# Optimization experiments

Hardware: AMD Instinct MI355X
Metric: run time of the kernel (lower is better)

The kernel has to match this reference:

```python
import jax, jax.numpy as jnp
import numpy as np
import math

IN_FEATURES = 4096
OUT_FEATURES = 4096
NUM_COMPONENTS = 256
TWO_PI = 2.0 * math.pi


def setup_inputs() -> dict:
    key = jax.random.key(0)
    k1, k2, k3, k4 = jax.random.split(key, 4)
    x = jax.random.normal(k1, (4096, IN_FEATURES), dtype=jnp.float32)
    mus = jax.random.uniform(k2, (NUM_COMPONENTS, 2), dtype=jnp.float32)
    log_vars = -3.0 - jax.random.uniform(k3, (NUM_COMPONENTS, 2), dtype=jnp.float32)
    weights = jax.random.uniform(k4, (NUM_COMPONENTS,), dtype=jnp.float32) / NUM_COMPONENTS
    return {"x": x, "mus": mus, "log_vars": log_vars, "weights": weights}


def reference(x, mus, log_vars, weights):
    in_features = x.shape[1]
    x_in_idx = jnp.linspace(0.0, 1.0, in_features, dtype=jnp.float32)    # [I]
    x_out_idx = jnp.linspace(0.0, 1.0, OUT_FEATURES, dtype=jnp.float32)  # [O]
    vars_ = jnp.exp(log_vars)  # [M, 2]

    # Input-side Gaussian basis, fused with 1/sqrt(2*pi*var) and component weight: [I, M]
    d_in = (x_in_idx[:, None] - mus[None, :, 0]) ** 2
    G_in = jnp.exp(-d_in / (2.0 * vars_[None, :, 0])) / jnp.sqrt(TWO_PI * vars_[None, :, 0]) * weights[None, :]
    C = x @ G_in  # [B, M]

    # Output-side Gaussian pdf (Normal(mu1, sigma1).log_prob(x_out).exp()): [M, O]
    d_out = (x_out_idx[None, :] - mus[:, 1:2]) ** 2
    G_out = jnp.exp(-d_out / (2.0 * vars_[:, 1:2])) / jnp.sqrt(TWO_PI * vars_[:, 1:2])

    x_out = (C @ G_out) / (in_features * jnp.sum(weights))  # [B, O]
    return x_out
```

## Files before the change

### kernel.cpp

```cpp
#include <hip/hip_runtime.h>
#include <hip/hip_bf16.h>
#include <math.h>

#define IN_FEAT 4096
#define OUT_FEAT 4096
#define NCOMP 256
#define BATCH 4096
#define TWO_PI_F 6.28318530717958647692f

typedef __attribute__((ext_vector_type(8))) short short8;
typedef __attribute__((ext_vector_type(8))) __bf16 bf16x8;
typedef __attribute__((ext_vector_type(4))) float f32x4;
typedef __attribute__((ext_vector_type(16))) float f32x16;

__device__ __forceinline__ ushort f2b(float f) {
  union { float f; unsigned u; } v; v.f = f;
  unsigned r = (v.u + 0x7fffu + ((v.u >> 16) & 1u)) >> 16;
  return (ushort)r;
}

__device__ __forceinline__ float b2f(short s) {
  union { unsigned u; float f; } v; v.u = ((unsigned)(ushort)s) << 16;
  return v.f;
}

__device__ __forceinline__ bf16x8 ld_frag(const void* p) {
  short8 s = *(const short8*)p;
  return __builtin_bit_cast(bf16x8, s);
}

__device__ __forceinline__ bf16x8 cvt8f(float4 a, float4 b) {
  bf16x8 r;
  r[0] = (__bf16)a.x; r[1] = (__bf16)a.y; r[2] = (__bf16)a.z; r[3] = (__bf16)a.w;
  r[4] = (__bf16)b.x; r[5] = (__bf16)b.y; r[6] = (__bf16)b.z; r[7] = (__bf16)b.w;
  return r;
}

__device__ __forceinline__ void gload_lds16(const void* g, void* l) {
  __builtin_amdgcn_global_load_lds(
      (const __attribute__((address_space(1))) void*)g,
      (__attribute__((address_space(3))) void*)l, 16, 0, 0);
}

__global__ __launch_bounds__(256) void prep_kernel(
    const float* __restrict__ mus, const float* __restrict__ lvs,
    const float* __restrict__ w,
    ushort* __restrict__ Gt, ushort* __restrict__ GoT) {
  int idx = blockIdx.x * 256 + threadIdx.x;
  if (idx < NCOMP * IN_FEAT) {
    int m = idx >> 12, i = idx & (IN_FEAT - 1);
    float v = expf(lvs[2 * m]);
    float d = (float)i * (1.0f / (IN_FEAT - 1)) - mus[2 * m];
    float g = expf(-d * d * (0.5f / v)) * rsqrtf(TWO_PI_F * v) * w[m];
    Gt[idx] = f2b(g);
  } else {
    idx -= NCOMP * IN_FEAT;
    int o = idx >> 8, m = idx & (NCOMP - 1);
    float v = expf(lvs[2 * m + 1]);
    float d = (float)o * (1.0f / (OUT_FEAT - 1)) - mus[2 * m + 1];
    float g = expf(-d * d * (0.5f / v)) * rsqrtf(TWO_PI_F * v);
    GoT[idx] = f2b(g);
  }
}

template<int NS>
__global__ __launch_bounds__(512, 2) void gemm1_kernel(
    const float* __restrict__ x, const ushort* __restrict__ Gt,
    ushort* __restrict__ Cpart) {
  constexpr int KR = IN_FEAT / NS;
  constexpr int NT = KR / 32;
  __shared__ __align__(16) ushort Bs[NT * 8192];
  const int tid = threadIdx.x, wid = tid >> 6, lane = tid & 63;
  const int l15 = lane & 15, q = lane >> 4;
  const int m0 = blockIdx.x * 256;
  const int kb0 = blockIdx.y * KR;

  {
    const int brow = lane >> 2;
    const int bsw = (((lane & 3) ^ ((lane >> 3) & 3)) << 3);
    #pragma unroll
    for (int i = 0; i < 16; ++i) {
      int idx = wid * 16 + i;
      int seg = idx >> 4, nf = idx & 15;
      gload_lds16(&Gt[(size_t)(nf * 16 + brow) * IN_FEAT + kb0 + seg * 32 + bsw],
                  &Bs[seg * 8192 + nf * 512]);
    }
  }

  const int rb0 = m0 + wid * 32;
  const int rb1 = rb0 + 16;
  const float* xa = &x[(size_t)(rb0 + l15) * IN_FEAT + kb0 + q * 8];
  const float* xb = &x[(size_t)(rb1 + l15) * IN_FEAT + kb0 + q * 8];

  float4 P[4][4];
  #pragma unroll
  for (int s = 0; s < 4; ++s) {
    P[s][0] = *(const float4*)(xa + s * 32);
    P[s][1] = *(const float4*)(xa + s * 32 + 4);
    P[s][2] = *(const float4*)(xb + s * 32);
    P[s][3] = *(const float4*)(xb + s * 32 + 4);
  }

  __syncthreads();

  f32x4 acc0[16] = {}, acc1[16] = {};
  const int fswz = (q << 4) ^ (((l15 >> 1) & 3) << 4);

  #pragma unroll
  for (int t = 0; t < NT; ++t) {
    bf16x8 af0 = cvt8f(P[t & 3][0], P[t & 3][1]);
    bf16x8 af1 = cvt8f(P[t & 3][2], P[t & 3][3]);
    if (t + 4 < NT) {
      P[t & 3][0] = *(const float4*)(xa + (t + 4) * 32);
      P[t & 3][1] = *(const float4*)(xa + (t + 4) * 32 + 4);
      P[t & 3][2] = *(const float4*)(xb + (t + 4) * 32);
      P[t & 3][3] = *(const float4*)(xb + (t + 4) * 32 + 4);
    }
    const char* sb = (const char*)Bs + t * 16384;
    #pragma unroll
    for (int nf = 0; nf < 16; ++nf) {
      bf16x8 bf = ld_frag(sb + (nf * 16 + l15) * 64 + fswz);
      acc0[nf] = __builtin_amdgcn_mfma_f32_16x16x32_bf16(af0, bf, acc0[nf], 0, 0, 0);
      acc1[nf] = __builtin_amdgcn_mfma_f32_16x16x32_bf16(af1, bf, acc1[nf], 0, 0, 0);
    }
  }

  ushort* Cp = Cpart + (size_t)blockIdx.y * ((size_t)BATCH * NCOMP);
  #pragma unroll
  for (int nf = 0; nf < 16; ++nf)
    #pragma unroll
    for (int r = 0; r < 4; ++r) {
      int col = nf * 16 + l15;
      Cp[(size_t)(rb0 + q * 4 + r) * NCOMP + col] = f2b(acc0[nf][r]);
      Cp[(size_t)(rb1 + q * 4 + r) * NCOMP + col] = f2b(acc1[nf][r]);
    }
}

template<int NS>
__global__ __launch_bounds__(256) void reduce_kernel(ushort* __restrict__ Cp) {
  size_t i = ((size_t)blockIdx.x * 256 + threadIdx.x) * 8;
  float s[8] = {};
  #pragma unroll
  for (int p = 0; p < NS; ++p) {
    short8 v = *(const short8*)&Cp[(size_t)p * BATCH * NCOMP + i];
    #pragma unroll
    for (int e = 0; e < 8; ++e) s[e] += b2f(v[e]);
  }
  short8 hh;
  #pragma unroll
  for (int e = 0; e < 8; ++e) hh[e] = (short)f2b(s[e]);
  *(short8*)&Cp[i] = hh;
}

__global__ __launch_bounds__(256, 4) void gemm2_kernel(
    const ushort* __restrict__ Cb, const ushort* __restrict__ GoT,
    const float* __restrict__ w, float* __restrict__ out) {
  __shared__ __align__(16) ushort lds[2 * 8192];
  const int tid = threadIdx.x, wid = tid >> 6, lane = tid & 63;
  const int m0 = blockIdx.y * 128, n0 = blockIdx.x * 128;
  const int wr = (wid >> 1) * 64, wc = (wid & 1) * 64;
  const int r32 = lane & 31, h = lane >> 5;

  float4 wv = *(const float4*)&w[lane * 4];
  float s = wv.x + wv.y + wv.z + wv.w;
  #pragma unroll
  for (int off = 32; off > 0; off >>= 1) s += __shfl_xor(s, off);
  const float scale = 1.0f / ((float)IN_FEAT * s);

  const int brow = lane >> 2;
  const int bswz = (((lane & 3) ^ ((lane >> 3) & 3)) << 3);
  const int sw0 = (h << 4) ^ (((r32 >> 1) & 3) << 4);

  f32x16 acc[2][2] = {};

  #define STAGE2(buf, k0)                                                    \
    _Pragma("unroll")                                                        \
    for (int q2 = 0; q2 < 2; ++q2) {                                         \
      int c = wid * 2 + q2;                                                  \
      int row = c * 16 + brow;                                               \
      gload_lds16(&Cb[(size_t)(m0 + row) * NCOMP + (k0) + bswz],             \
                  &lds[(buf) * 8192 + c * 512]);                             \
      gload_lds16(&GoT[(size_t)(n0 + row) * NCOMP + (k0) + bswz],            \
                  &lds[(buf) * 8192 + 4096 + c * 512]);                      \
    }

  STAGE2(0, 0)
  __syncthreads();

  for (int t = 0; t < 8; ++t) {
    if (t < 7) STAGE2((t + 1) & 1, (t + 1) * 32)
    const char* base = (const char*)lds + (t & 1) * 16384;
    const char* Bb = base + 8192;
    #pragma unroll
    for (int s2 = 0; s2 < 2; ++s2) {
      const int off = sw0 ^ (s2 << 5);
      bf16x8 a0 = ld_frag(base + (wr + r32) * 64 + off);
      bf16x8 a1 = ld_frag(base + (wr + 32 + r32) * 64 + off);
      bf16x8 b0 = ld_frag(Bb + (wc + r32) * 64 + off);
      bf16x8 b1 = ld_frag(Bb + (wc + 32 + r32) * 64 + off);
      acc[0][0] = __builtin_amdgcn_mfma_f32_32x32x16_bf16(a0, b0, acc[0][0], 0, 0, 0);
      acc[0][1] = __builtin_amdgcn_mfma_f32_32x32x16_bf16(a0, b1, acc[0][1], 0, 0, 0);
      acc[1][0] = __builtin_amdgcn_mfma_f32_32x32x16_bf16(a1, b0, acc[1][0], 0, 0, 0);
      acc[1][1] = __builtin_amdgcn_mfma_f32_32x32x16_bf16(a1, b1, acc[1][1], 0, 0, 0);
    }
    __syncthreads();
  }
  #undef STAGE2

  #pragma unroll
  for (int mi = 0; mi < 2; ++mi)
    #pragma unroll
    for (int nj = 0; nj < 2; ++nj)
      #pragma unroll
      for (int g = 0; g < 16; ++g) {
        int row = m0 + wr + mi * 32 + (g & 3) + 8 * (g >> 2) + 4 * h;
        int col = n0 + wc + nj * 32 + r32;
        out[(size_t)row * OUT_FEAT + col] = acc[mi][nj][g] * scale;
      }
}

extern "C" void kernel_launch(void* const* d_in, const int* in_sizes, int n_in,
                              void* d_out, int out_size, void* d_ws, size_t ws_size,
                              hipStream_t stream) {
  const float* x   = (const float*)d_in[0];
  const float* mus = (const float*)d_in[1];
  const float* lvs = (const float*)d_in[2];
  const float* w   = (const float*)d_in[3];
  float* out = (float*)d_out;

  ushort* Gt  = (ushort*)d_ws;
  ushort* GoT = Gt  + (size_t)NCOMP * IN_FEAT;
  ushort* Cpart = GoT + (size_t)OUT_FEAT * NCOMP;

  prep_kernel<<<(NCOMP * IN_FEAT + OUT_FEAT * NCOMP) / 256, 256, 0, stream>>>(
      mus, lvs, w, Gt, GoT);

  gemm1_kernel<16><<<dim3(BATCH / 256, 16), 512, 0, stream>>>(x, Gt, Cpart);
  reduce_kernel<16><<<BATCH * NCOMP / 8 / 256, 256, 0, stream>>>(Cpart);

  gemm2_kernel<<<dim3(OUT_FEAT / 128, BATCH / 128), 256, 0, stream>>>(
      Cpart, GoT, w, out);
}
```

Baseline: 65.19 us.

## Restructure gemm1 into 64-row tiles with fewer K splits and chunked B staging

The first GEMM now uses 64-row blocks, with each wave handling 16 rows and half of the 256 components. It loops over K in 256-wide chunks, staging G into LDS per chunk under barriers. The split-K factor drops from 16 to 4, or to 1 when the workspace is small, which cuts the partial-sum traffic and reduce work. The cost is less reuse of each staged G tile across rows and exposed load latency, since loads and compute are not double-buffered.

```diff
diff --git a/kernel.cpp b/kernel.cpp
--- a/kernel.cpp
+++ b/kernel.cpp
@@ -63,76 +63,70 @@
   }
 }
 
-template<int NS>
+template<int NSPLIT>
 __global__ __launch_bounds__(512, 2) void gemm1_kernel(
     const float* __restrict__ x, const ushort* __restrict__ Gt,
     ushort* __restrict__ Cpart) {
-  constexpr int KR = IN_FEAT / NS;
-  constexpr int NT = KR / 32;
-  __shared__ __align__(16) ushort Bs[NT * 8192];
+  constexpr int KR = IN_FEAT / NSPLIT;
+  constexpr int NSC = KR / 256;
+  __shared__ __align__(16) ushort Bs[8 * 8192];
   const int tid = threadIdx.x, wid = tid >> 6, lane = tid & 63;
   const int l15 = lane & 15, q = lane >> 4;
-  const int m0 = blockIdx.x * 256;
+  const int rg = wid >> 1, h2 = wid & 1;
+  const int m0 = blockIdx.x * 64;
   const int kb0 = blockIdx.y * KR;
 
-  {
-    const int brow = lane >> 2;
-    const int bsw = (((lane & 3) ^ ((lane >> 3) & 3)) << 3);
-    #pragma unroll
-    for (int i = 0; i < 16; ++i) {
-      int idx = wid * 16 + i;
-      int seg = idx >> 4, nf = idx & 15;
-      gload_lds16(&Gt[(size_t)(nf * 16 + brow) * IN_FEAT + kb0 + seg * 32 + bsw],
-                  &Bs[seg * 8192 + nf * 512]);
-    }
-  }
-
-  const int rb0 = m0 + wid * 32;
-  const int rb1 = rb0 + 16;
-  const float* xa = &x[(size_t)(rb0 + l15) * IN_FEAT + kb0 + q * 8];
-  const float* xb = &x[(size_t)(rb1 + l15) * IN_FEAT + kb0 + q * 8];
-
-  float4 P[4][4];
-  #pragma unroll
-  for (int s = 0; s < 4; ++s) {
-    P[s][0] = *(const float4*)(xa + s * 32);
-    P[s][1] = *(const float4*)(xa + s * 32 + 4);
-    P[s][2] = *(const float4*)(xb + s * 32);
-    P[s][3] = *(const float4*)(xb + s * 32 + 4);
-  }
-
-  __syncthreads();
-
-  f32x4 acc0[16] = {}, acc1[16] = {};
+  const int brow = lane >> 2;
+  const int bsw = (((lane & 3) ^ ((lane >> 3) & 3)) << 3);
   const int fswz = (q << 4) ^ (((l15 >> 1) & 3) << 4);
 
-  #pragma unroll
-  for (int t = 0; t < NT; ++t) {
-    bf16x8 af0 = cvt8f(P[t & 3][0], P[t & 3][1]);
-    bf16x8 af1 = cvt8f(P[t & 3][2], P[t & 3][3]);
-    if (t + 4 < NT) {
-      P[t & 3][0] = *(const float4*)(xa + (t + 4) * 32);
-      P[t & 3][1] = *(const float4*)(xa + (t + 4) * 32 + 4);
-      P[t & 3][2] = *(const float4*)(xb + (t + 4) * 32);
-      P[t & 3][3] = *(const float4*)(xb + (t + 4) * 32 + 4);
-    }
-    const char* sb = (const char*)Bs + t * 16384;
-    #pragma unroll
-    for (int nf = 0; nf < 16; ++nf) {
-      bf16x8 bf = ld_frag(sb + (nf * 16 + l15) * 64 + fswz);
-      acc0[nf] = __builtin_amdgcn_mfma_f32_16x16x32_bf16(af0, bf, acc0[nf], 0, 0, 0);
-      acc1[nf] = __builtin_amdgcn_mfma_f32_16x16x32_bf16(af1, bf, acc1[nf], 0, 0, 0);
+  const float* xa = &x[(size_t)(m0 + rg * 16 + l15) * IN_FEAT + kb0 + q * 8];
+
+  f32x4 acc[8] = {};
+  float4 P[4][2];
+
+  for (int kc = 0; kc < NSC; ++kc) {
+    if (kc) __builtin_amdgcn_s_barrier();
+    #pragma unroll
+    for (int nf = 0; nf < 16; ++nf)
+      gload_lds16(
+          &Gt[(size_t)(nf * 16 + brow) * IN_FEAT + kb0 + kc * 256 + wid * 32 + bsw],
+          &Bs[wid * 8192 + nf * 512]);
+    __builtin_amdgcn_sched_barrier(0);
+    const float* xk = xa + kc * 256;
+    #pragma unroll
+    for (int s = 0; s < 4; ++s) {
+      P[s][0] = *(const float4*)(xk + s * 32);
+      P[s][1] = *(const float4*)(xk + s * 32 + 4);
+    }
+    asm volatile("s_waitcnt vmcnt(8)" ::: "memory");
+    __builtin_amdgcn_s_barrier();
+    __builtin_amdgcn_sched_barrier(0);
+
+    #pragma unroll
+    for (int t = 0; t < 8; ++t) {
+      bf16x8 a = cvt8f(P[t & 3][0], P[t & 3][1]);
+      if (t < 4) {
+        P[t][0] = *(const float4*)(xk + (t + 4) * 32);
+        P[t][1] = *(const float4*)(xk + (t + 4) * 32 + 4);
+      }
+      const char* sb = (const char*)Bs + t * 16384;
+      #pragma unroll
+      for (int j = 0; j < 8; ++j) {
+        bf16x8 b = ld_frag(sb + ((h2 * 8 + j) * 16 + l15) * 64 + fswz);
+        acc[j] = __builtin_amdgcn_mfma_f32_16x16x32_bf16(a, b, acc[j], 0, 0, 0);
+      }
     }
   }
 
   ushort* Cp = Cpart + (size_t)blockIdx.y * ((size_t)BATCH * NCOMP);
   #pragma unroll
-  for (int nf = 0; nf < 16; ++nf)
+  for (int j = 0; j < 8; ++j)
     #pragma unroll
     for (int r = 0; r < 4; ++r) {
-      int col = nf * 16 + l15;
-      Cp[(size_t)(rb0 + q * 4 + r) * NCOMP + col] = f2b(acc0[nf][r]);
-      Cp[(size_t)(rb1 + q * 4 + r) * NCOMP + col] = f2b(acc1[nf][r]);
+      int row = m0 + rg * 16 + q * 4 + r;
+      int col = h2 * 128 + j * 16 + l15;
+      Cp[(size_t)row * NCOMP + col] = f2b(acc[j][r]);
     }
 }
 
@@ -232,11 +226,18 @@
   ushort* GoT = Gt  + (size_t)NCOMP * IN_FEAT;
   ushort* Cpart = GoT + (size_t)OUT_FEAT * NCOMP;
 
+  const size_t MiB = 1024 * 1024;
+  const bool split4 = ws_size >= 14 * MiB;
+
   prep_kernel<<<(NCOMP * IN_FEAT + OUT_FEAT * NCOMP) / 256, 256, 0, stream>>>(
       mus, lvs, w, Gt, GoT);
 
-  gemm1_kernel<16><<<dim3(BATCH / 256, 16), 512, 0, stream>>>(x, Gt, Cpart);
-  reduce_kernel<16><<<BATCH * NCOMP / 8 / 256, 256, 0, stream>>>(Cpart);
+  if (split4) {
+    gemm1_kernel<4><<<dim3(BATCH / 64, 4), 512, 0, stream>>>(x, Gt, Cpart);
+    reduce_kernel<4><<<BATCH * NCOMP / 8 / 256, 256, 0, stream>>>(Cpart);
+  } else {
+    gemm1_kernel<1><<<dim3(BATCH / 64, 1), 512, 0, stream>>>(x, Gt, Cpart);
+  }
 
   gemm2_kernel<<<dim3(OUT_FEAT / 128, BATCH / 128), 256, 0, stream>>>(
       Cpart, GoT, w, out);
```

Result: faster. 61.34 us (median of 2 runs) (-5.9%).

## Restructure gemm1 to small row tiles with LDS-staged x and double-buffered Gt

Applied to the files above, without the earlier changes.

Gemm1 now covers 32 batch rows per block instead of 256 and splits K four ways instead of sixteen. Each block converts its x slice to bf16 once into swizzled LDS, then streams Gt chunks through a double-buffered LDS pipeline. Each wave owns 32 output columns. This cuts the partial-sum buffer and the reduce traffic and gives more blocks. In exchange Gt is re-read by every row block, and the large LDS footprint (64KB x tile plus 64KB Gt buffers) limits occupancy to one block per CU. The split4 branch is dead, since both paths launch the same kernels.

```diff
diff --git a/kernel.cpp b/kernel.cpp
--- a/kernel.cpp
+++ b/kernel.cpp
@@ -29,11 +29,11 @@
   return __builtin_bit_cast(bf16x8, s);
 }
 
-__device__ __forceinline__ bf16x8 cvt8f(float4 a, float4 b) {
+__device__ __forceinline__ short8 cvt8s(float4 a, float4 b) {
   bf16x8 r;
   r[0] = (__bf16)a.x; r[1] = (__bf16)a.y; r[2] = (__bf16)a.z; r[3] = (__bf16)a.w;
   r[4] = (__bf16)b.x; r[5] = (__bf16)b.y; r[6] = (__bf16)b.z; r[7] = (__bf16)b.w;
-  return r;
+  return __builtin_bit_cast(short8, r);
 }
 
 __device__ __forceinline__ void gload_lds16(const void* g, void* l) {
@@ -64,76 +64,92 @@
 }
 
 template<int NS>
-__global__ __launch_bounds__(512, 2) void gemm1_kernel(
+__global__ __launch_bounds__(512, 1) void gemm1_kernel(
     const float* __restrict__ x, const ushort* __restrict__ Gt,
     ushort* __restrict__ Cpart) {
   constexpr int KR = IN_FEAT / NS;
-  constexpr int NT = KR / 32;
-  __shared__ __align__(16) ushort Bs[NT * 8192];
+  constexpr int NCH = KR / 64;
+  __shared__ __align__(16) ushort xs[32 * (KR > 1024 ? 1024 : KR)];
+  __shared__ __align__(16) ushort Bs[2 * 16384];
   const int tid = threadIdx.x, wid = tid >> 6, lane = tid & 63;
   const int l15 = lane & 15, q = lane >> 4;
-  const int m0 = blockIdx.x * 256;
+  const int m0 = blockIdx.x * 32;
   const int kb0 = blockIdx.y * KR;
 
+  const int brow = lane >> 2;
+  const int bsw = (((lane & 3) ^ ((lane >> 3) & 3)) << 3);
+
+  #define STAGE_B(buf, kc)                                                   \
+    _Pragma("unroll")                                                        \
+    for (int i_ = 0; i_ < 4; ++i_) {                                         \
+      int idx_ = wid * 4 + i_, seg_ = idx_ >> 4, nf_ = idx_ & 15;            \
+      gload_lds16(&Gt[(size_t)(nf_ * 16 + brow) * IN_FEAT + kb0 +            \
+                      (kc) * 64 + seg_ * 32 + bsw],                          \
+                  &Bs[(buf) * 16384 + seg_ * 8192 + nf_ * 512]);             \
+    }
+
+  STAGE_B(0, 0)
+
   {
-    const int brow = lane >> 2;
-    const int bsw = (((lane & 3) ^ ((lane >> 3) & 3)) << 3);
-    #pragma unroll
-    for (int i = 0; i < 16; ++i) {
-      int idx = wid * 16 + i;
-      int seg = idx >> 4, nf = idx & 15;
-      gload_lds16(&Gt[(size_t)(nf * 16 + brow) * IN_FEAT + kb0 + seg * 32 + bsw],
-                  &Bs[seg * 8192 + nf * 512]);
-    }
-  }
-
-  const int rb0 = m0 + wid * 32;
-  const int rb1 = rb0 + 16;
-  const float* xa = &x[(size_t)(rb0 + l15) * IN_FEAT + kb0 + q * 8];
-  const float* xb = &x[(size_t)(rb1 + l15) * IN_FEAT + kb0 + q * 8];
-
-  float4 P[4][4];
-  #pragma unroll
-  for (int s = 0; s < 4; ++s) {
-    P[s][0] = *(const float4*)(xa + s * 32);
-    P[s][1] = *(const float4*)(xa + s * 32 + 4);
-    P[s][2] = *(const float4*)(xb + s * 32);
-    P[s][3] = *(const float4*)(xb + s * 32 + 4);
-  }
-
+    constexpr int NP = KR / 512;
+    float4 F0[4 * NP], F1[4 * NP];
+    #pragma unroll
+    for (int i = 0; i < 4 * NP; ++i) {
+      int r = wid * 4 + (i >> (NP == 2 ? 1 : 0)) % 4;
+      int pass = (NP == 2) ? (i & 1) : (i & (NP - 1));
+      r = wid * 4 + i / NP;
+      pass = i % NP;
+      const float* src = &x[(size_t)(m0 + r) * IN_FEAT + kb0 + pass * 512 + lane * 8];
+      F0[i] = *(const float4*)src;
+      F1[i] = *(const float4*)(src + 4);
+    }
+    #pragma unroll
+    for (int i = 0; i < 4 * NP; ++i) {
+      int r = wid * 4 + i / NP;
+      int pass = i % NP;
+      int byte = (r * (KR * 2) + pass * 1024 + lane * 16) ^ ((r & 7) << 4);
+      *(short8*)((char*)xs + byte) = cvt8s(F0[i], F1[i]);
+    }
+  }
   __syncthreads();
 
-  f32x4 acc0[16] = {}, acc1[16] = {};
+  f32x4 acc[2][2] = {};
   const int fswz = (q << 4) ^ (((l15 >> 1) & 3) << 4);
-
-  #pragma unroll
-  for (int t = 0; t < NT; ++t) {
-    bf16x8 af0 = cvt8f(P[t & 3][0], P[t & 3][1]);
-    bf16x8 af1 = cvt8f(P[t & 3][2], P[t & 3][3]);
-    if (t + 4 < NT) {
-      P[t & 3][0] = *(const float4*)(xa + (t + 4) * 32);
-      P[t & 3][1] = *(const float4*)(xa + (t + 4) * 32 + 4);
-      P[t & 3][2] = *(const float4*)(xb + (t + 4) * 32);
-      P[t & 3][3] = *(const float4*)(xb + (t + 4) * 32 + 4);
-    }
-    const char* sb = (const char*)Bs + t * 16384;
-    #pragma unroll
-    for (int nf = 0; nf < 16; ++nf) {
-      bf16x8 bf = ld_frag(sb + (nf * 16 + l15) * 64 + fswz);
-      acc0[nf] = __builtin_amdgcn_mfma_f32_16x16x32_bf16(af0, bf, acc0[nf], 0, 0, 0);
-      acc1[nf] = __builtin_amdgcn_mfma_f32_16x16x32_bf16(af1, bf, acc1[nf], 0, 0, 0);
-    }
-  }
+  const int aswz0 = (l15 & 7) << 4;
+
+  for (int kc = 0; kc < NCH; ++kc) {
+    if (kc + 1 < NCH) STAGE_B((kc + 1) & 1, kc + 1)
+    const char* bb = (const char*)Bs + (kc & 1) * 32768;
+    #pragma unroll
+    for (int ks = 0; ks < 2; ++ks) {
+      const int kbyte = kc * 128 + ks * 64 + q * 16;
+      bf16x8 a0 = ld_frag((const char*)xs +
+                          (((l15) * (KR * 2)) + (kbyte ^ aswz0)));
+      bf16x8 a1 = ld_frag((const char*)xs +
+                          (((16 + l15) * (KR * 2)) + (kbyte ^ aswz0)));
+      const char* sb = bb + ks * 16384;
+      bf16x8 b0 = ld_frag(sb + ((wid * 2 + 0) * 16 + l15) * 64 + fswz);
+      bf16x8 b1 = ld_frag(sb + ((wid * 2 + 1) * 16 + l15) * 64 + fswz);
+      acc[0][0] = __builtin_amdgcn_mfma_f32_16x16x32_bf16(a0, b0, acc[0][0], 0, 0, 0);
+      acc[0][1] = __builtin_amdgcn_mfma_f32_16x16x32_bf16(a0, b1, acc[0][1], 0, 0, 0);
+      acc[1][0] = __builtin_amdgcn_mfma_f32_16x16x32_bf16(a1, b0, acc[1][0], 0, 0, 0);
+      acc[1][1] = __builtin_amdgcn_mfma_f32_16x16x32_bf16(a1, b1, acc[1][1], 0, 0, 0);
+    }
+    __syncthreads();
+  }
+  #undef STAGE_B
 
   ushort* Cp = Cpart + (size_t)blockIdx.y * ((size_t)BATCH * NCOMP);
   #pragma unroll
-  for (int nf = 0; nf < 16; ++nf)
-    #pragma unroll
-    for (int r = 0; r < 4; ++r) {
-      int col = nf * 16 + l15;
-      Cp[(size_t)(rb0 + q * 4 + r) * NCOMP + col] = f2b(acc0[nf][r]);
-      Cp[(size_t)(rb1 + q * 4 + r) * NCOMP + col] = f2b(acc1[nf][r]);
-    }
+  for (int mi = 0; mi < 2; ++mi)
+    #pragma unroll
+    for (int nj = 0; nj < 2; ++nj)
+      #pragma unroll
+      for (int r = 0; r < 4; ++r) {
+        int row = m0 + mi * 16 + q * 4 + r;
+        int col = wid * 32 + nj * 16 + l15;
+        Cp[(size_t)row * NCOMP + col] = f2b(acc[mi][nj][r]);
+      }
 }
 
 template<int NS>
@@ -232,11 +248,19 @@
   ushort* GoT = Gt  + (size_t)NCOMP * IN_FEAT;
   ushort* Cpart = GoT + (size_t)OUT_FEAT * NCOMP;
 
+  const size_t MiB = 1024 * 1024;
+  const bool split4 = ws_size >= 12 * MiB;
+
   prep_kernel<<<(NCOMP * IN_FEAT + OUT_FEAT * NCOMP) / 256, 256, 0, stream>>>(
       mus, lvs, w, Gt, GoT);
 
-  gemm1_kernel<16><<<dim3(BATCH / 256, 16), 512, 0, stream>>>(x, Gt, Cpart);
-  reduce_kernel<16><<<BATCH * NCOMP / 8 / 256, 256, 0, stream>>>(Cpart);
+  if (split4) {
+    gemm1_kernel<4><<<dim3(BATCH / 32, 4), 512, 0, stream>>>(x, Gt, Cpart);
+    reduce_kernel<4><<<BATCH * NCOMP / 8 / 256, 256, 0, stream>>>(Cpart);
+  } else {
+    gemm1_kernel<4><<<dim3(BATCH / 32, 4), 512, 0, stream>>>(x, Gt, Cpart);
+    reduce_kernel<4><<<BATCH * NCOMP / 8 / 256, 256, 0, stream>>>(Cpart);
+  }
 
   gemm2_kernel<<<dim3(OUT_FEAT / 128, BATCH / 128), 256, 0, stream>>>(
       Cpart, GoT, w, out);
```

New measurement: 77.67 us. 1.19x slower.
